# Optimization experiments

Measured on AMD Instinct MI355X. Metric: run time of the kernel, lower is better.

## Reference

```python
import jax, jax.numpy as jnp
import numpy as np

# AlphaFold-style Invariant Point Attention (the StructureModule's core op)
N, SD, PD, C, H, PQ, PV = 768, 384, 128, 16, 12, 4, 8
W_C = (2.0 / (9.0 * PQ)) ** 0.5   # point-distance weight
W_L = (1.0 / 3.0) ** 0.5          # logit balancing weight
INV_SQRT_C = C ** -0.5


def setup_inputs() -> dict:
    key = jax.random.key(0)
    ks = jax.random.split(key, 11)
    single_rep = jax.random.normal(ks[0], (N, SD), jnp.float32)
    pair_rep = jax.random.normal(ks[1], (N, N, PD), jnp.float32)
    # random rigid frames: proper orthonormal rotations via QR + translations
    M = jax.random.normal(ks[2], (N, 3, 3), jnp.float32)
    frames_R, _ = jnp.linalg.qr(M)
    frames_t = jax.random.normal(ks[3], (N, 3), jnp.float32) * 10.0
    s = 0.02
    W_qkv = jax.random.normal(ks[4], (SD, 3 * H * C), jnp.float32) * s
    W_b = jax.random.normal(ks[5], (PD, H), jnp.float32) * s
    W_qkp = jax.random.normal(ks[6], (SD, 2 * H * PQ * 3), jnp.float32) * s
    W_vp = jax.random.normal(ks[7], (SD, H * PV * 3), jnp.float32) * s
    gamma = jnp.zeros((H,), jnp.float32)
    W_out = jax.random.normal(ks[8], (H * (PD + C + 3 * PV + PV), SD), jnp.float32) * s
    b_out = jnp.zeros((SD,), jnp.float32)
    return dict(single_rep=single_rep, pair_rep=pair_rep, frames_R=frames_R,
                frames_t=frames_t, W_qkv=W_qkv, W_b=W_b, W_qkp=W_qkp,
                W_vp=W_vp, gamma=gamma, W_out=W_out, b_out=b_out)


def reference(single_rep, pair_rep, frames_R, frames_t,
              W_qkv, W_b, W_qkp, W_vp, gamma, W_out, b_out):
    n = single_rep.shape[0]
    # scalar q/k/v: [n, C, H] (module views as (proj_dim, n_heads))
    q, k, v = [x.reshape(n, C, H) for x in jnp.split(single_rep @ W_qkv, 3, axis=-1)]
    b = jnp.einsum('ijd,dh->ijh', pair_rep, W_b)             # pair bias [n,n,H]
    qp, kp = [x.reshape(n, PQ, 3, H) for x in jnp.split(single_rep @ W_qkp, 2, axis=-1)]
    vp = (single_rep @ W_vp).reshape(n, PV, 3, H)

    def to_global(p):  # apply frame T_i = (R_i, t_i) to local points
        return jnp.einsum('nxy,npyh->npxh', frames_R, p) + frames_t[:, None, :, None]

    qg, kg, vg = to_global(qp), to_global(kp), to_global(vp)

    # squared distances sum_p ||T_i q_p - T_j k_p||^2 without [n,n,PQ,3,H] temp
    sq = jnp.sum(qg * qg, axis=(1, 2))                       # [n,H]
    sk = jnp.sum(kg * kg, axis=(1, 2))                       # [n,H]
    cross = jnp.einsum('ipxh,jpxh->ijh', qg, kg)             # [n,n,H]
    dist2 = sq[:, None, :] + sk[None, :, :] - 2.0 * cross

    head_w = jax.nn.softplus(gamma)                          # per-head gamma
    logits = W_L * (INV_SQRT_C * jnp.einsum('ich,jch->ijh', q, k)
                    + b - 0.5 * W_C * head_w * dist2)
    attn = jax.nn.softmax(logits, axis=1)                    # softmax over j

    o_pair = jnp.einsum('ijh,ijd->ihd', attn, pair_rep)      # [n,H,PD]
    o = jnp.einsum('ijh,jch->ihc', attn, v)                  # [n,H,C]
    og = jnp.einsum('ijh,jpxh->ipxh', attn, vg)              # [n,PV,3,H]
    # back to local frame: R_i^T (og - t_i)
    ol = jnp.einsum('nyx,npyh->npxh', frames_R, og - frames_t[:, None, :, None])
    onorm = jnp.sqrt(jnp.sum(ol * ol, axis=2) + 1e-8)        # [n,PV,H]

    feats = jnp.concatenate([
        o_pair.reshape(n, -1),
        o.reshape(n, -1),
        jnp.moveaxis(ol, -1, 1).reshape(n, -1),
        jnp.moveaxis(onorm, -1, 1).reshape(n, -1)], axis=-1)  # [n, H*(PD+C+3PV+PV)]
    return feats @ W_out + b_out
```

## Files before the change

### kernel.cpp

```cpp
#include <hip/hip_runtime.h>
#include <hip/hip_bf16.h>

typedef float v4f __attribute__((ext_vector_type(4)));
typedef short bf8 __attribute__((ext_vector_type(8)));
typedef unsigned short u16;

constexpr float W_C_ = 0.23570226039551584f;
constexpr float W_L_ = 0.5773502691896258f;

__device__ __forceinline__ u16 f2bf(float f) {
  unsigned u = __float_as_uint(f);
  return (u16)((u + 0x7FFFu + ((u >> 16) & 1u)) >> 16);
}
__device__ __forceinline__ float bf2f(u16 h) {
  return __uint_as_float(((unsigned)h) << 16);
}
__device__ __forceinline__ float dot4(v4f a, v4f b) {
  return a.x * b.x + a.y * b.y + a.z * b.z + a.w * b.w;
}

__global__ __launch_bounds__(256) void convert_bf(const float* __restrict__ src,
                                                  u16* __restrict__ dst, int n8) {
  int idx = blockIdx.x * 256 + threadIdx.x;
  if (idx < n8) {
    v4f a = ((const v4f*)src)[idx * 2];
    v4f b = ((const v4f*)src)[idx * 2 + 1];
    bf8 o;
    o[0] = (short)f2bf(a.x); o[1] = (short)f2bf(a.y);
    o[2] = (short)f2bf(a.z); o[3] = (short)f2bf(a.w);
    o[4] = (short)f2bf(b.x); o[5] = (short)f2bf(b.y);
    o[6] = (short)f2bf(b.z); o[7] = (short)f2bf(b.w);
    ((bf8*)dst)[idx] = o;
  }
}

__global__ __launch_bounds__(256) void wfrag_k(const float* __restrict__ W,
                                               u16* __restrict__ frag,
                                               int K, int N) {
  __shared__ float Ws[32 * 384];
  const int ks = blockIdx.x, k0 = ks * 32, t = threadIdx.x;
  const int NTfull = (N + 15) >> 4;
  for (int n0 = 0; n0 < N; n0 += 384) {
    int PN = N - n0; if (PN > 384) PN = 384;
    __syncthreads();
    for (int idx = t; idx < 32 * PN; idx += 256) {
      int r = idx / PN, c = idx - r * PN;
      Ws[r * PN + c] = W[(size_t)(k0 + r) * N + n0 + c];
    }
    __syncthreads();
    int NTp = (PN + 15) >> 4;
    for (int c = t; c < NTp * 64; c += 256) {
      int nt = c >> 6, l = c & 63;
      int col = nt * 16 + (l & 15);
      bf8 o;
#pragma unroll
      for (int e = 0; e < 8; e++) {
        int rr = (l >> 4) * 8 + e;
        float f = (col < PN) ? Ws[rr * PN + col] : 0.f;
        o[e] = (short)f2bf(f);
      }
      ((bf8*)frag)[((size_t)ks * NTfull + (n0 >> 4) + nt) * 64 + l] = o;
    }
  }
}

__global__ __launch_bounds__(256) void gemm_f32(
    const float* __restrict__ A, const float* __restrict__ B,
    float* __restrict__ C, int M, int N, int K) {
  __shared__ float AsT[32][68];
  __shared__ float Bs[32][36];
  const int bi = blockIdx.y * 64, bj = blockIdx.x * 32;
  const int t = threadIdx.x, ty = t >> 4, tx = t & 15;
  v4f acc0 = {0.f, 0.f, 0.f, 0.f}, acc1 = {0.f, 0.f, 0.f, 0.f};
  for (int k0 = 0; k0 < K; k0 += 32) {
#pragma unroll
    for (int q = 0; q < 2; q++) {
      int idx = t + 256 * q;
      int row = idx >> 3, c4 = idx & 7;
      v4f av = *(const v4f*)(A + (size_t)(bi + row) * K + k0 + c4 * 4);
      AsT[c4 * 4 + 0][row] = av.x;
      AsT[c4 * 4 + 1][row] = av.y;
      AsT[c4 * 4 + 2][row] = av.z;
      AsT[c4 * 4 + 3][row] = av.w;
    }
    {
      int r = t >> 3, c4 = t & 7;
      *(v4f*)&Bs[r][c4 * 4] = *(const v4f*)(B + (size_t)(k0 + r) * N + bj + c4 * 4);
    }
    __syncthreads();
#pragma unroll
    for (int kk = 0; kk < 32; kk++) {
      v4f a = *(const v4f*)&AsT[kk][ty * 4];
      float b0 = Bs[kk][tx * 2], b1 = Bs[kk][tx * 2 + 1];
      acc0 += a * b0;
      acc1 += a * b1;
    }
    __syncthreads();
  }
#pragma unroll
  for (int e = 0; e < 4; e++) {
    int row = bi + ty * 4 + e;
    C[(size_t)row * N + bj + tx * 2] = acc0[e];
    C[(size_t)row * N + bj + tx * 2 + 1] = acc1[e];
  }
}

__global__ __launch_bounds__(256) void mfma_gemm(
    const u16* __restrict__ Abf, const u16* __restrict__ Bfrag,
    const float* __restrict__ bias, float* __restrict__ C,
    int M, int N, int K, int ldc) {
  __shared__ u16 As[64 * 32];
  const int t = threadIdx.x, w = t >> 6, l = t & 63;
  const int bi = blockIdx.y * 64, nt0 = blockIdx.x * 2;
  const int NT = N >> 4, KS = K >> 5;
  v4f acc0 = {0.f, 0.f, 0.f, 0.f}, acc1 = {0.f, 0.f, 0.f, 0.f};
  const int srow = t >> 2, sc = t & 3;
  const int wslot = (sc ^ (srow & 3)) * 8;
  const bf8* Bf = (const bf8*)Bfrag;

  bf8 areg = *(const bf8*)(Abf + (size_t)(bi + srow) * K + sc * 8);
  bf8 b0 = Bf[(size_t)(0 * NT + nt0) * 64 + l];
  bf8 b1 = Bf[(size_t)(0 * NT + nt0 + 1) * 64 + l];
  const int rdoff = (w * 16 + (l & 15)) * 32 + (((l >> 4) ^ (l & 3)) * 8);
  for (int ks = 0; ks < KS; ks++) {
    *(bf8*)&As[srow * 32 + wslot] = areg;
    bf8 an, bn0, bn1;
    if (ks + 1 < KS) {
      an = *(const bf8*)(Abf + (size_t)(bi + srow) * K + (ks + 1) * 32 + sc * 8);
      bn0 = Bf[(size_t)((ks + 1) * NT + nt0) * 64 + l];
      bn1 = Bf[(size_t)((ks + 1) * NT + nt0 + 1) * 64 + l];
    }
    __syncthreads();
    bf8 af = *(const bf8*)&As[rdoff];
    acc0 = __builtin_amdgcn_mfma_f32_16x16x32_bf16(af, b0, acc0, 0, 0, 0);
    acc1 = __builtin_amdgcn_mfma_f32_16x16x32_bf16(af, b1, acc1, 0, 0, 0);
    __syncthreads();
    areg = an; b0 = bn0; b1 = bn1;
  }
  int col0 = nt0 * 16 + (l & 15), col1 = col0 + 16;
  float bb0 = bias ? bias[col0] : 0.f;
  float bb1 = bias ? bias[col1] : 0.f;
#pragma unroll
  for (int r = 0; r < 4; r++) {
    int row = bi + w * 16 + (l >> 4) * 4 + r;
    C[(size_t)row * ldc + col0] = acc0[r] + bb0;
    C[(size_t)row * ldc + col1] = acc1[r] + bb1;
  }
}

__global__ __launch_bounds__(256) void prep_kernel(
    const float* __restrict__ projQKV, const float* __restrict__ projQKP,
    const float* __restrict__ projVP, const float* __restrict__ fR,
    const float* __restrict__ ft,
    float* __restrict__ qbuf, float* __restrict__ v2buf,
    float* __restrict__ qgbuf, float* __restrict__ sqbuf,
    float* __restrict__ kTT) {
  const int n = blockIdx.x, t = threadIdx.x;
  __shared__ float R[9], tt[3];
  __shared__ float qgL[144], kgL[144];
  if (t < 9) R[t] = fR[n * 9 + t];
  if (t < 3) tt[t] = ft[n * 3 + t];
  __syncthreads();
  const float* rQKV = projQKV + (size_t)n * 576;
  const float* rQKP = projQKP + (size_t)n * 288;
  const float* rVP = projVP + (size_t)n * 288;
  if (t < 192) {
    int h = t >> 4, c = t & 15;
    qbuf[(size_t)n * 192 + t] = rQKV[c * 12 + h];
    kTT[(size_t)(h * 29 + c) * 768 + n] = rQKV[192 + c * 12 + h];
    v2buf[(size_t)n * 480 + h * 40 + c] = rQKV[384 + c * 12 + h];
  }
  if (t < 144) {
    int e = t / 12, h = t % 12;
    int p = e / 3, x = e % 3;
    float aq = tt[x], ak = tt[x];
#pragma unroll
    for (int y = 0; y < 3; y++) {
      float r = R[x * 3 + y];
      aq += r * rQKP[p * 36 + y * 12 + h];
      ak += r * rQKP[144 + p * 36 + y * 12 + h];
    }
    qgL[h * 12 + e] = aq;
    kgL[h * 12 + e] = ak;
    qgbuf[(size_t)n * 144 + h * 12 + e] = aq;
    kTT[(size_t)(h * 29 + 16 + e) * 768 + n] = ak;
  }
  for (int idx = t; idx < 288; idx += 256) {
    int e = idx / 12, h = idx % 12;
    int p = e / 3, x = e % 3;
    float a = tt[x];
#pragma unroll
    for (int y = 0; y < 3; y++) a += R[x * 3 + y] * rVP[p * 36 + y * 12 + h];
    v2buf[(size_t)n * 480 + h * 40 + 16 + e] = a;
  }
  __syncthreads();
  if (t < 12) {
    float s = 0.f;
#pragma unroll
    for (int e = 0; e < 12; e++) { float v = qgL[t * 12 + e]; s += v * v; }
    sqbuf[n * 12 + t] = s;
  } else if (t < 24) {
    int h = t - 12;
    float s = 0.f;
#pragma unroll
    for (int e = 0; e < 12; e++) { float v = kgL[h * 12 + e]; s += v * v; }
    kTT[(size_t)(h * 29 + 28) * 768 + n] = s;
  }
}

__global__ __launch_bounds__(256) void bias_mfma(
    const float* __restrict__ pair, const u16* __restrict__ WbFrag,
    u16* __restrict__ bbuf) {
  const int jt = blockIdx.x, i = blockIdx.y;
  const int t = threadIdx.x, w = t >> 6, l = t & 63;
  __shared__ u16 pS[64 * 128];
  bf8 bf[4];
  const bf8* Wf = (const bf8*)WbFrag;
#pragma unroll
  for (int ks = 0; ks < 4; ks++) bf[ks] = Wf[ks * 64 + l];
  const float* pg = pair + ((size_t)i * 768 + jt * 64) * 128;
#pragma unroll
  for (int it = 0; it < 4; it++) {
    int idx = t + 256 * it;
    int j = idx >> 4, c = idx & 15;
    v4f x0 = *(const v4f*)(pg + j * 128 + c * 8);
    v4f x1 = *(const v4f*)(pg + j * 128 + c * 8 + 4);
    bf8 pk;
    pk[0] = (short)f2bf(x0.x); pk[1] = (short)f2bf(x0.y);
    pk[2] = (short)f2bf(x0.z); pk[3] = (short)f2bf(x0.w);
    pk[4] = (short)f2bf(x1.x); pk[5] = (short)f2bf(x1.y);
    pk[6] = (short)f2bf(x1.z); pk[7] = (short)f2bf(x1.w);
    *(bf8*)&pS[j * 128 + ((c ^ (j & 15)) * 8)] = pk;
  }
  __syncthreads();
  v4f acc = {0.f, 0.f, 0.f, 0.f};
#pragma unroll
  for (int ks = 0; ks < 4; ks++) {
    int slot = (ks * 4 + (l >> 4)) ^ (l & 15);
    bf8 af = *(const bf8*)&pS[(w * 16 + (l & 15)) * 128 + slot * 8];
    acc = __builtin_amdgcn_mfma_f32_16x16x32_bf16(af, bf[ks], acc, 0, 0, 0);
  }
  int h = l & 15;
  if (h < 12) {
    int jbase = jt * 64 + w * 16 + (l >> 4) * 4;
    u16* dst = bbuf + ((size_t)i * 12 + h) * 768 + jbase;
#pragma unroll
    for (int r = 0; r < 4; r++) dst[r] = f2bf(acc[r]);
  }
}

__global__ __launch_bounds__(256) void qk_softmax(
    const float* __restrict__ qbuf, const float* __restrict__ qgbuf,
    const float* __restrict__ sqbuf, const float* __restrict__ kTT,
    const u16* __restrict__ bbuf, const float* __restrict__ gamma,
    u16* __restrict__ attn) {
  const int h = blockIdx.x, i = blockIdx.y, t = threadIdx.x;
  __shared__ float red[8];
  float q[16], qg[12];
  const float* qb = qbuf + (size_t)i * 192 + h * 16;
  const float* qgb = qgbuf + (size_t)i * 144 + h * 12;
#pragma unroll
  for (int c = 0; c < 16; c++) q[c] = qb[c];
#pragma unroll
  for (int e = 0; e < 12; e++) qg[e] = qgb[e];
  float sq = sqbuf[i * 12 + h];
  float g = gamma[h];
  float hw = fmaxf(g, 0.f) + log1pf(expf(-fabsf(g)));
  const float* kb = kTT + (size_t)h * 29 * 768;
  const u16* brow = bbuf + ((size_t)i * 12 + h) * 768;
  float lg[3];
#pragma unroll
  for (int s = 0; s < 3; s++) {
    int j = t + 256 * s;
    float qk = 0.f;
#pragma unroll
    for (int c = 0; c < 16; c++) qk += q[c] * kb[c * 768 + j];
    float cr = 0.f;
#pragma unroll
    for (int e = 0; e < 12; e++) cr += qg[e] * kb[(16 + e) * 768 + j];
    float sk = kb[28 * 768 + j];
    float b = bf2f(brow[j]);
    float d2 = sq + sk - 2.f * cr;
    lg[s] = W_L_ * (0.25f * qk + b - 0.5f * W_C_ * hw * d2);
  }
  float m = fmaxf(fmaxf(lg[0], lg[1]), lg[2]);
#pragma unroll
  for (int o = 32; o >= 1; o >>= 1) m = fmaxf(m, __shfl_xor(m, o));
  if ((t & 63) == 0) red[t >> 6] = m;
  __syncthreads();
  m = fmaxf(fmaxf(red[0], red[1]), fmaxf(red[2], red[3]));
  float p0 = __expf(lg[0] - m), p1 = __expf(lg[1] - m), p2 = __expf(lg[2] - m);
  float ss = p0 + p1 + p2;
#pragma unroll
  for (int o = 32; o >= 1; o >>= 1) ss += __shfl_xor(ss, o);
  if ((t & 63) == 0) red[4 + (t >> 6)] = ss;
  __syncthreads();
  float inv = 1.f / (red[4] + red[5] + red[6] + red[7]);
  u16* arow = attn + ((size_t)i * 12 + h) * 768;
  arow[t] = f2bf(p0 * inv);
  arow[t + 256] = f2bf(p1 * inv);
  arow[t + 512] = f2bf(p2 * inv);
}

__global__ __launch_bounds__(256) void opair_k(
    const float* __restrict__ pair, const u16* __restrict__ attn,
    u16* __restrict__ feats_bf) {
  const int i = blockIdx.x, t = threadIdx.x;
  const int w = t >> 6, l = t & 63;
  const int dq = l & 31, hh = l >> 5;
  __shared__ float pairL[64][132];
  __shared__ float ALf[12][68];
  v4f acc[6];
#pragma unroll
  for (int k = 0; k < 6; k++) acc[k] = (v4f){0.f, 0.f, 0.f, 0.f};

  v4f pr[8];
  bf8 areg;
  {
    const float* pg = pair + ((size_t)i * 768) * 128;
#pragma unroll
    for (int it = 0; it < 8; it++) {
      int idx = t + 256 * it;
      pr[it] = *(const v4f*)(pg + (idx >> 5) * 128 + (idx & 31) * 4);
    }
    if (t < 96)
      areg = *(const bf8*)(attn + ((size_t)i * 12 + (t >> 3)) * 768 + (t & 7) * 8);
  }
  for (int jt = 0; jt < 12; jt++) {
#pragma unroll
    for (int it = 0; it < 8; it++) {
      int idx = t + 256 * it;
      *(v4f*)&pairL[idx >> 5][(idx & 31) * 4] = pr[it];
    }
    if (t < 96) {
      int hA = t >> 3, c = t & 7;
#pragma unroll
      for (int e = 0; e < 8; e++) ALf[hA][c * 8 + e] = bf2f((u16)areg[e]);
    }
    if (jt < 11) {
      const float* pg = pair + ((size_t)i * 768 + (jt + 1) * 64) * 128;
#pragma unroll
      for (int it = 0; it < 8; it++) {
        int idx = t + 256 * it;
        pr[it] = *(const v4f*)(pg + (idx >> 5) * 128 + (idx & 31) * 4);
      }
      if (t < 96)
        areg = *(const bf8*)(attn + ((size_t)i * 12 + (t >> 3)) * 768 +
                             (jt + 1) * 64 + (t & 7) * 8);
    }
    __syncthreads();
#pragma unroll
    for (int jj16 = 0; jj16 < 16; jj16++) {
      int jj = w * 16 + jj16;
      v4f pv = *(const v4f*)&pairL[jj][dq * 4];
      float a0 = ALf[hh * 6 + 0][jj];
      float a1 = ALf[hh * 6 + 1][jj];
      float a2 = ALf[hh * 6 + 2][jj];
      float a3 = ALf[hh * 6 + 3][jj];
      float a4 = ALf[hh * 6 + 4][jj];
      float a5 = ALf[hh * 6 + 5][jj];
      acc[0] += pv * a0; acc[1] += pv * a1; acc[2] += pv * a2;
      acc[3] += pv * a3; acc[4] += pv * a4; acc[5] += pv * a5;
    }
    __syncthreads();
  }
  float* red = &pairL[0][0];
#pragma unroll
  for (int k = 0; k < 6; k++)
    *(v4f*)&red[((w * 12 + hh * 6 + k) << 7) + dq * 4] = acc[k];
  __syncthreads();
  const size_t fb = (size_t)i * 2112;
#pragma unroll
  for (int s = 0; s < 6; s++) {
    int o = t + 256 * s;
    int ho = o >> 7, dd = o & 127;
    float v = red[(ho << 7) + dd] + red[((12 + ho) << 7) + dd] +
              red[((24 + ho) << 7) + dd] + red[((36 + ho) << 7) + dd];
    feats_bf[fb + o] = f2bf(v);
  }
}

__global__ __launch_bounds__(256) void ov_k(
    const u16* __restrict__ attn, const float* __restrict__ v2buf,
    float* __restrict__ O2) {
  const int i0 = blockIdx.x * 64, h = blockIdx.y, t = threadIdx.x;
  __shared__ float AL[64][65];
  __shared__ float VL[64][48];
  const int il = t & 63, eb = (t >> 6) * 12;
  v4f acc0 = {0.f, 0.f, 0.f, 0.f}, acc1 = {0.f, 0.f, 0.f, 0.f},
      acc2 = {0.f, 0.f, 0.f, 0.f};
  for (int jt = 0; jt < 12; ++jt) {
    const int j0 = jt * 64;
#pragma unroll
    for (int q = 0; q < 2; q++) {
      int idx = t + 256 * q;
      int ii = idx >> 3, c = idx & 7;
      bf8 av = *(const bf8*)(attn + ((size_t)(i0 + ii) * 12 + h) * 768 + j0 + c * 8);
#pragma unroll
      for (int e = 0; e < 8; e++) AL[ii][c * 8 + e] = bf2f((u16)av[e]);
    }
#pragma unroll
    for (int q = 0; q < 3; q++) {
      int idx = t + q * 256;
      if (idx < 640) {
        int jj = idx / 10, e4 = idx % 10;
        *(v4f*)&VL[jj][e4 * 4] =
            *(const v4f*)(v2buf + (size_t)(j0 + jj) * 480 + h * 40 + e4 * 4);
      }
    }
    __syncthreads();
#pragma unroll 4
    for (int jj = 0; jj < 64; ++jj) {
      float a = AL[il][jj];
      v4f v0 = *(const v4f*)&VL[jj][eb];
      v4f v1 = *(const v4f*)&VL[jj][eb + 4];
      v4f v2 = *(const v4f*)&VL[jj][eb + 8];
      acc0 += v0 * a;
      acc1 += v1 * a;
      acc2 += v2 * a;
    }
    __syncthreads();
  }
  float* orow = O2 + ((size_t)(i0 + il) * 12 + h) * 40;
#pragma unroll
  for (int s = 0; s < 12; ++s) {
    int e = eb + s;
    if (e < 40) {
      float v = (s < 4) ? ((float*)&acc0)[s]
                        : (s < 8) ? ((float*)&acc1)[s - 4] : ((float*)&acc2)[s - 8];
      orow[e] = v;
    }
  }
}

__global__ __launch_bounds__(256) void finalize_k(
    const float* __restrict__ O2, const float* __restrict__ fR,
    const float* __restrict__ ft, u16* __restrict__ feats_bf) {
  const int i = blockIdx.x, t = threadIdx.x;
  __shared__ float RL[9], ttL[3];
  if (t < 9) RL[t] = fR[i * 9 + t];
  if (t < 3) ttL[t] = ft[i * 3 + t];
  __syncthreads();
  const float* orow = O2 + (size_t)i * 480;
  const size_t fb = (size_t)i * 2112;
  if (t < 192) {
    int h = t >> 4, c = t & 15;
    feats_bf[fb + 1536 + h * 16 + c] = f2bf(orow[h * 40 + c]);
  }
  if (t < 96) {
    int h = t >> 3, p = t & 7;
    float og0 = orow[h * 40 + 16 + p * 3 + 0] - ttL[0];
    float og1 = orow[h * 40 + 16 + p * 3 + 1] - ttL[1];
    float og2 = orow[h * 40 + 16 + p * 3 + 2] - ttL[2];
    float o0 = RL[0] * og0 + RL[3] * og1 + RL[6] * og2;
    float o1 = RL[1] * og0 + RL[4] * og1 + RL[7] * og2;
    float o2 = RL[2] * og0 + RL[5] * og1 + RL[8] * og2;
    feats_bf[fb + 1728 + h * 24 + p * 3 + 0] = f2bf(o0);
    feats_bf[fb + 1728 + h * 24 + p * 3 + 1] = f2bf(o1);
    feats_bf[fb + 1728 + h * 24 + p * 3 + 2] = f2bf(o2);
    feats_bf[fb + 2016 + h * 8 + p] = f2bf(sqrtf(o0 * o0 + o1 * o1 + o2 * o2 + 1e-8f));
  }
}

extern "C" void kernel_launch(void* const* d_in, const int* in_sizes, int n_in,
                              void* d_out, int out_size, void* d_ws, size_t ws_size,
                              hipStream_t stream) {
  const float* single = (const float*)d_in[0];
  const float* pair = (const float*)d_in[1];
  const float* fR = (const float*)d_in[2];
  const float* ft = (const float*)d_in[3];
  const float* W_qkv = (const float*)d_in[4];
  const float* W_b = (const float*)d_in[5];
  const float* W_qkp = (const float*)d_in[6];
  const float* W_vp = (const float*)d_in[7];
  const float* gamma = (const float*)d_in[8];
  const float* W_out = (const float*)d_in[9];
  const float* b_out = (const float*)d_in[10];
  float* out = (float*)d_out;

  float* ws = (float*)d_ws;
  float* projQKV = ws;
  float* projQKP = projQKV + 442368;
  float* projVP  = projQKP + 221184;
  float* qbuf    = projVP + 221184;
  float* v2buf   = qbuf + 147456;
  float* qgbuf   = v2buf + 368640;
  float* sqbuf   = qgbuf + 110592;
  float* kTT     = sqbuf + 9216;
  float* O2      = kTT + 267264;
  u16* single_bf = (u16*)(O2 + 368640);
  u16* WqkvFrag  = single_bf + 294912;
  u16* WbFrag    = WqkvFrag + 221184;
  u16* WoutFrag  = WbFrag + 2048;
  u16* bbuf      = WoutFrag + 811008;
  u16* attn      = bbuf + 7077888;
  u16* feats_bf  = attn + 7077888;

  convert_bf<<<144, 256, 0, stream>>>(single, single_bf, 36864);
  wfrag_k<<<12, 256, 0, stream>>>(W_qkv, WqkvFrag, 384, 576);
  wfrag_k<<<4, 256, 0, stream>>>(W_b, WbFrag, 128, 12);
  wfrag_k<<<66, 256, 0, stream>>>(W_out, WoutFrag, 2112, 384);
  gemm_f32<<<dim3(9, 12), 256, 0, stream>>>(single, W_qkp, projQKP, 768, 288, 384);
  gemm_f32<<<dim3(9, 12), 256, 0, stream>>>(single, W_vp, projVP, 768, 288, 384);
  mfma_gemm<<<dim3(18, 12), 256, 0, stream>>>(single_bf, WqkvFrag, nullptr,
                                              projQKV, 768, 576, 384, 576);
  prep_kernel<<<768, 256, 0, stream>>>(projQKV, projQKP, projVP, fR, ft,
                                       qbuf, v2buf, qgbuf, sqbuf, kTT);
  bias_mfma<<<dim3(12, 768), 256, 0, stream>>>(pair, WbFrag, bbuf);
  qk_softmax<<<dim3(12, 768), 256, 0, stream>>>(qbuf, qgbuf, sqbuf, kTT, bbuf,
                                                gamma, attn);
  opair_k<<<768, 256, 0, stream>>>(pair, attn, feats_bf);
  ov_k<<<dim3(12, 12), 256, 0, stream>>>(attn, v2buf, O2);
  finalize_k<<<768, 256, 0, stream>>>(O2, fR, ft, feats_bf);
  mfma_gemm<<<dim3(12, 12), 256, 0, stream>>>(feats_bf, WoutFrag, b_out,
                                              out, 768, 384, 2112, 384);
}
```

Before: 310.6 us.

## Fuse pair bias with QK logits, cache bf16 pair copy, split softmax

The bias kernel now also computes the full logits (scalar QK, point-distance terms) per 64-column tile and writes them as fp32, while emitting a bf16 copy of pair_rep. A separate row softmax kernel then turns logits into bf16 attention, and opair reads the bf16 pair copy instead of re-reading fp32 pair. This halves the second large pair read in exchange for an extra bf16 write plus an fp32 logits round-trip. The point projections also move from fp32 SIMT GEMMs to bf16 MFMA GEMMs, which adds rounding error to the geometric terms.

```diff
diff --git a/kernel.cpp b/kernel.cpp
--- a/kernel.cpp
+++ b/kernel.cpp
@@ -36,7 +36,7 @@
 
 __global__ __launch_bounds__(256) void wfrag_k(const float* __restrict__ W,
                                                u16* __restrict__ frag,
-                                               int K, int N) {
+                                               int K, int N, float scale) {
   __shared__ float Ws[32 * 384];
   const int ks = blockIdx.x, k0 = ks * 32, t = threadIdx.x;
   const int NTfull = (N + 15) >> 4;
@@ -56,52 +56,11 @@
 #pragma unroll
       for (int e = 0; e < 8; e++) {
         int rr = (l >> 4) * 8 + e;
-        float f = (col < PN) ? Ws[rr * PN + col] : 0.f;
+        float f = (col < PN) ? Ws[rr * PN + col] * scale : 0.f;
         o[e] = (short)f2bf(f);
       }
       ((bf8*)frag)[((size_t)ks * NTfull + (n0 >> 4) + nt) * 64 + l] = o;
     }
-  }
-}
-
-__global__ __launch_bounds__(256) void gemm_f32(
-    const float* __restrict__ A, const float* __restrict__ B,
-    float* __restrict__ C, int M, int N, int K) {
-  __shared__ float AsT[32][68];
-  __shared__ float Bs[32][36];
-  const int bi = blockIdx.y * 64, bj = blockIdx.x * 32;
-  const int t = threadIdx.x, ty = t >> 4, tx = t & 15;
-  v4f acc0 = {0.f, 0.f, 0.f, 0.f}, acc1 = {0.f, 0.f, 0.f, 0.f};
-  for (int k0 = 0; k0 < K; k0 += 32) {
-#pragma unroll
-    for (int q = 0; q < 2; q++) {
-      int idx = t + 256 * q;
-      int row = idx >> 3, c4 = idx & 7;
-      v4f av = *(const v4f*)(A + (size_t)(bi + row) * K + k0 + c4 * 4);
-      AsT[c4 * 4 + 0][row] = av.x;
-      AsT[c4 * 4 + 1][row] = av.y;
-      AsT[c4 * 4 + 2][row] = av.z;
-      AsT[c4 * 4 + 3][row] = av.w;
-    }
-    {
-      int r = t >> 3, c4 = t & 7;
-      *(v4f*)&Bs[r][c4 * 4] = *(const v4f*)(B + (size_t)(k0 + r) * N + bj + c4 * 4);
-    }
-    __syncthreads();
-#pragma unroll
-    for (int kk = 0; kk < 32; kk++) {
-      v4f a = *(const v4f*)&AsT[kk][ty * 4];
-      float b0 = Bs[kk][tx * 2], b1 = Bs[kk][tx * 2 + 1];
-      acc0 += a * b0;
-      acc1 += a * b1;
-    }
-    __syncthreads();
-  }
-#pragma unroll
-  for (int e = 0; e < 4; e++) {
-    int row = bi + ty * 4 + e;
-    C[(size_t)row * N + bj + tx * 2] = acc0[e];
-    C[(size_t)row * N + bj + tx * 2 + 1] = acc1[e];
   }
 }
 
@@ -152,9 +111,9 @@
     const float* __restrict__ projQKV, const float* __restrict__ projQKP,
     const float* __restrict__ projVP, const float* __restrict__ fR,
     const float* __restrict__ ft,
-    float* __restrict__ qbuf, float* __restrict__ v2buf,
-    float* __restrict__ qgbuf, float* __restrict__ sqbuf,
-    float* __restrict__ kTT) {
+    float* __restrict__ qbuf, float* __restrict__ kbuf, float* __restrict__ v2buf,
+    float* __restrict__ qgbuf, float* __restrict__ kgbuf,
+    float* __restrict__ sqbuf, float* __restrict__ skbuf) {
   const int n = blockIdx.x, t = threadIdx.x;
   __shared__ float R[9], tt[3];
   __shared__ float qgL[144], kgL[144];
@@ -167,7 +126,7 @@
   if (t < 192) {
     int h = t >> 4, c = t & 15;
     qbuf[(size_t)n * 192 + t] = rQKV[c * 12 + h];
-    kTT[(size_t)(h * 29 + c) * 768 + n] = rQKV[192 + c * 12 + h];
+    kbuf[(size_t)n * 192 + t] = rQKV[192 + c * 12 + h];
     v2buf[(size_t)n * 480 + h * 40 + c] = rQKV[384 + c * 12 + h];
   }
   if (t < 144) {
@@ -183,7 +142,7 @@
     qgL[h * 12 + e] = aq;
     kgL[h * 12 + e] = ak;
     qgbuf[(size_t)n * 144 + h * 12 + e] = aq;
-    kTT[(size_t)(h * 29 + 16 + e) * 768 + n] = ak;
+    kgbuf[(size_t)n * 144 + h * 12 + e] = ak;
   }
   for (int idx = t; idx < 288; idx += 256) {
     int e = idx / 12, h = idx % 12;
@@ -204,21 +163,38 @@
     float s = 0.f;
 #pragma unroll
     for (int e = 0; e < 12; e++) { float v = kgL[h * 12 + e]; s += v * v; }
-    kTT[(size_t)(h * 29 + 28) * 768 + n] = s;
-  }
-}
-
-__global__ __launch_bounds__(256) void bias_mfma(
+    skbuf[n * 12 + h] = s;
+  }
+}
+
+__global__ __launch_bounds__(256) void biaslogit_k(
     const float* __restrict__ pair, const u16* __restrict__ WbFrag,
-    u16* __restrict__ bbuf) {
+    const float* __restrict__ gamma,
+    const float* __restrict__ qbuf, const float* __restrict__ kbuf,
+    const float* __restrict__ qgbuf, const float* __restrict__ kgbuf,
+    const float* __restrict__ sqbuf, const float* __restrict__ skbuf,
+    u16* __restrict__ pair_bf, float* __restrict__ logits) {
   const int jt = blockIdx.x, i = blockIdx.y;
   const int t = threadIdx.x, w = t >> 6, l = t & 63;
   __shared__ u16 pS[64 * 128];
-  bf8 bf[4];
+  __shared__ float lgL[64 * 15];
+  __shared__ float qL[192], qgL[144], c1L[12], c2L[12];
+
+  if (t < 192) qL[t] = qbuf[(size_t)i * 192 + t];
+  if (t < 144) qgL[t] = qgbuf[(size_t)i * 144 + t];
+  if (t < 12) {
+    float g = gamma[t];
+    float hw = fmaxf(g, 0.f) + log1pf(expf(-fabsf(g)));
+    c1L[t] = W_L_ * W_C_ * hw;
+    c2L[t] = -0.5f * c1L[t] * sqbuf[i * 12 + t];
+  }
+  bf8 wb[4];
   const bf8* Wf = (const bf8*)WbFrag;
 #pragma unroll
-  for (int ks = 0; ks < 4; ks++) bf[ks] = Wf[ks * 64 + l];
+  for (int ks = 0; ks < 4; ks++) wb[ks] = Wf[ks * 64 + l];
+
   const float* pg = pair + ((size_t)i * 768 + jt * 64) * 128;
+  u16* pbg = pair_bf + ((size_t)i * 768 + jt * 64) * 128;
 #pragma unroll
   for (int it = 0; it < 4; it++) {
     int idx = t + 256 * it;
@@ -231,118 +207,136 @@
     pk[4] = (short)f2bf(x1.x); pk[5] = (short)f2bf(x1.y);
     pk[6] = (short)f2bf(x1.z); pk[7] = (short)f2bf(x1.w);
     *(bf8*)&pS[j * 128 + ((c ^ (j & 15)) * 8)] = pk;
-  }
-  __syncthreads();
-  v4f acc = {0.f, 0.f, 0.f, 0.f};
-#pragma unroll
-  for (int ks = 0; ks < 4; ks++) {
-    int slot = (ks * 4 + (l >> 4)) ^ (l & 15);
-    bf8 af = *(const bf8*)&pS[(w * 16 + (l & 15)) * 128 + slot * 8];
-    acc = __builtin_amdgcn_mfma_f32_16x16x32_bf16(af, bf[ks], acc, 0, 0, 0);
-  }
-  int h = l & 15;
-  if (h < 12) {
-    int jbase = jt * 64 + w * 16 + (l >> 4) * 4;
-    u16* dst = bbuf + ((size_t)i * 12 + h) * 768 + jbase;
-#pragma unroll
-    for (int r = 0; r < 4; r++) dst[r] = f2bf(acc[r]);
-  }
-}
-
-__global__ __launch_bounds__(256) void qk_softmax(
-    const float* __restrict__ qbuf, const float* __restrict__ qgbuf,
-    const float* __restrict__ sqbuf, const float* __restrict__ kTT,
-    const u16* __restrict__ bbuf, const float* __restrict__ gamma,
-    u16* __restrict__ attn) {
-  const int h = blockIdx.x, i = blockIdx.y, t = threadIdx.x;
-  __shared__ float red[8];
-  float q[16], qg[12];
-  const float* qb = qbuf + (size_t)i * 192 + h * 16;
-  const float* qgb = qgbuf + (size_t)i * 144 + h * 12;
-#pragma unroll
-  for (int c = 0; c < 16; c++) q[c] = qb[c];
-#pragma unroll
-  for (int e = 0; e < 12; e++) qg[e] = qgb[e];
-  float sq = sqbuf[i * 12 + h];
-  float g = gamma[h];
-  float hw = fmaxf(g, 0.f) + log1pf(expf(-fabsf(g)));
-  const float* kb = kTT + (size_t)h * 29 * 768;
-  const u16* brow = bbuf + ((size_t)i * 12 + h) * 768;
-  float lg[3];
+    *(bf8*)(pbg + j * 128 + c * 8) = pk;
+  }
+  __syncthreads();
+
+  {
+    v4f acc = {0.f, 0.f, 0.f, 0.f};
+#pragma unroll
+    for (int ks = 0; ks < 4; ks++) {
+      int slot = (ks * 4 + (l >> 4)) ^ (l & 15);
+      bf8 af = *(const bf8*)&pS[(w * 16 + (l & 15)) * 128 + slot * 8];
+      acc = __builtin_amdgcn_mfma_f32_16x16x32_bf16(af, wb[ks], acc, 0, 0, 0);
+    }
+    int h = l & 15;
+    if (h < 12) {
+#pragma unroll
+      for (int r = 0; r < 4; r++)
+        lgL[(w * 16 + (l >> 4) * 4 + r) * 15 + h] = acc[r];
+    }
+  }
+  __syncthreads();
+
+  {
+    const int j = t >> 2, hg = t & 3;
+    const int jg = jt * 64 + j;
+#pragma unroll
+    for (int hh = 0; hh < 3; hh++) {
+      int h = hg * 3 + hh;
+      const v4f* kk = (const v4f*)(kbuf + (size_t)jg * 192 + h * 16);
+      const v4f* qq = (const v4f*)&qL[h * 16];
+      float qk = dot4(kk[0], qq[0]) + dot4(kk[1], qq[1]) +
+                 dot4(kk[2], qq[2]) + dot4(kk[3], qq[3]);
+      const v4f* kg = (const v4f*)(kgbuf + (size_t)jg * 144 + h * 12);
+      const v4f* qg = (const v4f*)&qgL[h * 12];
+      float cr = dot4(kg[0], qg[0]) + dot4(kg[1], qg[1]) + dot4(kg[2], qg[2]);
+      float sk = skbuf[(size_t)jg * 12 + h];
+      lgL[j * 15 + h] += 0.25f * W_L_ * qk + c1L[h] * (cr - 0.5f * sk) + c2L[h];
+    }
+  }
+  __syncthreads();
+
 #pragma unroll
   for (int s = 0; s < 3; s++) {
-    int j = t + 256 * s;
-    float qk = 0.f;
-#pragma unroll
-    for (int c = 0; c < 16; c++) qk += q[c] * kb[c * 768 + j];
-    float cr = 0.f;
-#pragma unroll
-    for (int e = 0; e < 12; e++) cr += qg[e] * kb[(16 + e) * 768 + j];
-    float sk = kb[28 * 768 + j];
-    float b = bf2f(brow[j]);
-    float d2 = sq + sk - 2.f * cr;
-    lg[s] = W_L_ * (0.25f * qk + b - 0.5f * W_C_ * hw * d2);
-  }
-  float m = fmaxf(fmaxf(lg[0], lg[1]), lg[2]);
-#pragma unroll
-  for (int o = 32; o >= 1; o >>= 1) m = fmaxf(m, __shfl_xor(m, o));
-  if ((t & 63) == 0) red[t >> 6] = m;
-  __syncthreads();
-  m = fmaxf(fmaxf(red[0], red[1]), fmaxf(red[2], red[3]));
-  float p0 = __expf(lg[0] - m), p1 = __expf(lg[1] - m), p2 = __expf(lg[2] - m);
-  float ss = p0 + p1 + p2;
-#pragma unroll
-  for (int o = 32; o >= 1; o >>= 1) ss += __shfl_xor(ss, o);
-  if ((t & 63) == 0) red[4 + (t >> 6)] = ss;
-  __syncthreads();
-  float inv = 1.f / (red[4] + red[5] + red[6] + red[7]);
-  u16* arow = attn + ((size_t)i * 12 + h) * 768;
-  arow[t] = f2bf(p0 * inv);
-  arow[t + 256] = f2bf(p1 * inv);
-  arow[t + 512] = f2bf(p2 * inv);
+    int o = t + 256 * s;
+    int h = o >> 6, j = o & 63;
+    logits[((size_t)i * 12 + h) * 768 + jt * 64 + j] = lgL[j * 15 + h];
+  }
+}
+
+__global__ __launch_bounds__(256) void softmax_bf(const float* __restrict__ L,
+                                                  u16* __restrict__ attn) {
+  const int row = blockIdx.x * 4 + (threadIdx.x >> 6);
+  const int lane = threadIdx.x & 63;
+  const v4f* p = (const v4f*)(L + (size_t)row * 768);
+  v4f a0 = p[lane], a1 = p[lane + 64], a2 = p[lane + 128];
+  float m0 = fmaxf(fmaxf(a0.x, a0.y), fmaxf(a0.z, a0.w));
+  float m1 = fmaxf(fmaxf(a1.x, a1.y), fmaxf(a1.z, a1.w));
+  float m2 = fmaxf(fmaxf(a2.x, a2.y), fmaxf(a2.z, a2.w));
+  float m = fmaxf(m0, fmaxf(m1, m2));
+#pragma unroll
+  for (int s = 32; s >= 1; s >>= 1) m = fmaxf(m, __shfl_xor(m, s));
+  a0.x = __expf(a0.x - m); a0.y = __expf(a0.y - m);
+  a0.z = __expf(a0.z - m); a0.w = __expf(a0.w - m);
+  a1.x = __expf(a1.x - m); a1.y = __expf(a1.y - m);
+  a1.z = __expf(a1.z - m); a1.w = __expf(a1.w - m);
+  a2.x = __expf(a2.x - m); a2.y = __expf(a2.y - m);
+  a2.z = __expf(a2.z - m); a2.w = __expf(a2.w - m);
+  float s = a0.x + a0.y + a0.z + a0.w + a1.x + a1.y + a1.z + a1.w +
+            a2.x + a2.y + a2.z + a2.w;
+#pragma unroll
+  for (int q = 32; q >= 1; q >>= 1) s += __shfl_xor(s, q);
+  float inv = 1.f / s;
+  a0 *= inv; a1 *= inv; a2 *= inv;
+  u16* arow = attn + (size_t)row * 768;
+  uint2 pk;
+  pk.x = (unsigned)f2bf(a0.x) | ((unsigned)f2bf(a0.y) << 16);
+  pk.y = (unsigned)f2bf(a0.z) | ((unsigned)f2bf(a0.w) << 16);
+  *(uint2*)&arow[lane * 4] = pk;
+  pk.x = (unsigned)f2bf(a1.x) | ((unsigned)f2bf(a1.y) << 16);
+  pk.y = (unsigned)f2bf(a1.z) | ((unsigned)f2bf(a1.w) << 16);
+  *(uint2*)&arow[256 + lane * 4] = pk;
+  pk.x = (unsigned)f2bf(a2.x) | ((unsigned)f2bf(a2.y) << 16);
+  pk.y = (unsigned)f2bf(a2.z) | ((unsigned)f2bf(a2.w) << 16);
+  *(uint2*)&arow[512 + lane * 4] = pk;
 }
 
 __global__ __launch_bounds__(256) void opair_k(
-    const float* __restrict__ pair, const u16* __restrict__ attn,
+    const u16* __restrict__ pair_bf, const u16* __restrict__ attn,
     u16* __restrict__ feats_bf) {
   const int i = blockIdx.x, t = threadIdx.x;
   const int w = t >> 6, l = t & 63;
   const int dq = l & 31, hh = l >> 5;
-  __shared__ float pairL[64][132];
-  __shared__ float ALf[12][68];
+  __shared__ float smemf[6160];
+  u16* pS = (u16*)smemf;
+  float* ALf = smemf + 4096;
+  float* red = smemf;
+
   v4f acc[6];
 #pragma unroll
   for (int k = 0; k < 6; k++) acc[k] = (v4f){0.f, 0.f, 0.f, 0.f};
 
-  v4f pr[8];
+  bf8 pr[4];
   bf8 areg;
   {
-    const float* pg = pair + ((size_t)i * 768) * 128;
-#pragma unroll
-    for (int it = 0; it < 8; it++) {
+    const u16* pg = pair_bf + (size_t)i * 768 * 128;
+#pragma unroll
+    for (int it = 0; it < 4; it++) {
       int idx = t + 256 * it;
-      pr[it] = *(const v4f*)(pg + (idx >> 5) * 128 + (idx & 31) * 4);
+      pr[it] = *(const bf8*)(pg + (idx >> 4) * 128 + (idx & 15) * 8);
     }
     if (t < 96)
       areg = *(const bf8*)(attn + ((size_t)i * 12 + (t >> 3)) * 768 + (t & 7) * 8);
   }
   for (int jt = 0; jt < 12; jt++) {
 #pragma unroll
-    for (int it = 0; it < 8; it++) {
+    for (int it = 0; it < 4; it++) {
       int idx = t + 256 * it;
-      *(v4f*)&pairL[idx >> 5][(idx & 31) * 4] = pr[it];
+      int j = idx >> 4, c = idx & 15;
+      *(bf8*)&pS[j * 128 + ((c ^ (j & 15)) * 8)] = pr[it];
     }
     if (t < 96) {
       int hA = t >> 3, c = t & 7;
 #pragma unroll
-      for (int e = 0; e < 8; e++) ALf[hA][c * 8 + e] = bf2f((u16)areg[e]);
+      for (int e = 0; e < 8; e++) ALf[hA * 68 + c * 8 + e] = bf2f((u16)areg[e]);
     }
     if (jt < 11) {
-      const float* pg = pair + ((size_t)i * 768 + (jt + 1) * 64) * 128;
-#pragma unroll
-      for (int it = 0; it < 8; it++) {
+      const u16* pg = pair_bf + ((size_t)i * 768 + (jt + 1) * 64) * 128;
+#pragma unroll
+      for (int it = 0; it < 4; it++) {
         int idx = t + 256 * it;
-        pr[it] = *(const v4f*)(pg + (idx >> 5) * 128 + (idx & 31) * 4);
+        pr[it] = *(const bf8*)(pg + (idx >> 4) * 128 + (idx & 15) * 8);
       }
       if (t < 96)
         areg = *(const bf8*)(attn + ((size_t)i * 12 + (t >> 3)) * 768 +
@@ -352,30 +346,32 @@
 #pragma unroll
     for (int jj16 = 0; jj16 < 16; jj16++) {
       int jj = w * 16 + jj16;
-      v4f pv = *(const v4f*)&pairL[jj][dq * 4];
-      float a0 = ALf[hh * 6 + 0][jj];
-      float a1 = ALf[hh * 6 + 1][jj];
-      float a2 = ALf[hh * 6 + 2][jj];
-      float a3 = ALf[hh * 6 + 3][jj];
-      float a4 = ALf[hh * 6 + 4][jj];
-      float a5 = ALf[hh * 6 + 5][jj];
+      const u16* pv4 = &pS[jj * 128 + (((dq >> 1) ^ (jj & 15)) * 8) + (dq & 1) * 4];
+      v4f pv;
+      pv.x = bf2f(pv4[0]); pv.y = bf2f(pv4[1]);
+      pv.z = bf2f(pv4[2]); pv.w = bf2f(pv4[3]);
+      float a0 = ALf[(hh * 6 + 0) * 68 + jj];
+      float a1 = ALf[(hh * 6 + 1) * 68 + jj];
+      float a2 = ALf[(hh * 6 + 2) * 68 + jj];
+      float a3 = ALf[(hh * 6 + 3) * 68 + jj];
+      float a4 = ALf[(hh * 6 + 4) * 68 + jj];
+      float a5 = ALf[(hh * 6 + 5) * 68 + jj];
       acc[0] += pv * a0; acc[1] += pv * a1; acc[2] += pv * a2;
       acc[3] += pv * a3; acc[4] += pv * a4; acc[5] += pv * a5;
     }
     __syncthreads();
   }
-  float* red = &pairL[0][0];
 #pragma unroll
   for (int k = 0; k < 6; k++)
-    *(v4f*)&red[((w * 12 + hh * 6 + k) << 7) + dq * 4] = acc[k];
+    *(v4f*)&red[(w * 12 + hh * 6 + k) * 128 + dq * 4] = acc[k];
   __syncthreads();
   const size_t fb = (size_t)i * 2112;
 #pragma unroll
   for (int s = 0; s < 6; s++) {
     int o = t + 256 * s;
     int ho = o >> 7, dd = o & 127;
-    float v = red[(ho << 7) + dd] + red[((12 + ho) << 7) + dd] +
-              red[((24 + ho) << 7) + dd] + red[((36 + ho) << 7) + dd];
+    float v = red[ho * 128 + dd] + red[(12 + ho) * 128 + dd] +
+              red[(24 + ho) * 128 + dd] + red[(36 + ho) * 128 + dd];
     feats_bf[fb + o] = f2bf(v);
   }
 }
@@ -480,36 +476,47 @@
 
   float* ws = (float*)d_ws;
   float* projQKV = ws;
-  float* projQKP = projQKV + 442368;
-  float* projVP  = projQKP + 221184;
-  float* qbuf    = projVP + 221184;
-  float* v2buf   = qbuf + 147456;
-  float* qgbuf   = v2buf + 368640;
-  float* sqbuf   = qgbuf + 110592;
-  float* kTT     = sqbuf + 9216;
-  float* O2      = kTT + 267264;
-  u16* single_bf = (u16*)(O2 + 368640);
-  u16* WqkvFrag  = single_bf + 294912;
-  u16* WbFrag    = WqkvFrag + 221184;
-  u16* WoutFrag  = WbFrag + 2048;
-  u16* bbuf      = WoutFrag + 811008;
-  u16* attn      = bbuf + 7077888;
-  u16* feats_bf  = attn + 7077888;
+  float* projQKP = ws + 442368;
+  float* projVP  = ws + 663552;
+  float* qbuf    = ws + 884736;
+  float* kbuf    = ws + 1032192;
+  float* v2buf   = ws + 1179648;
+  float* qgbuf   = ws + 1548288;
+  float* kgbuf   = ws + 1658880;
+  float* sqbuf   = ws + 1769472;
+  float* skbuf   = ws + 1778688;
+  float* logits  = ws + 1787904;
+  float* O2      = ws + 8865792;
+  u16* ub        = (u16*)(ws + 9234432);
+  u16* single_bf = ub;
+  u16* WqkvFrag  = ub + 294912;
+  u16* WqkpFrag  = ub + 516096;
+  u16* WvpFrag   = ub + 626688;
+  u16* WbFrag    = ub + 737280;
+  u16* WoutFrag  = ub + 739328;
+  u16* attn      = ub + 1550336;
+  u16* feats_bf  = ub + 8628224;
+  u16* pair_bf   = ub + 10250240;
 
   convert_bf<<<144, 256, 0, stream>>>(single, single_bf, 36864);
-  wfrag_k<<<12, 256, 0, stream>>>(W_qkv, WqkvFrag, 384, 576);
-  wfrag_k<<<4, 256, 0, stream>>>(W_b, WbFrag, 128, 12);
-  wfrag_k<<<66, 256, 0, stream>>>(W_out, WoutFrag, 2112, 384);
-  gemm_f32<<<dim3(9, 12), 256, 0, stream>>>(single, W_qkp, projQKP, 768, 288, 384);
-  gemm_f32<<<dim3(9, 12), 256, 0, stream>>>(single, W_vp, projVP, 768, 288, 384);
+  wfrag_k<<<12, 256, 0, stream>>>(W_qkv, WqkvFrag, 384, 576, 1.f);
+  wfrag_k<<<12, 256, 0, stream>>>(W_qkp, WqkpFrag, 384, 288, 1.f);
+  wfrag_k<<<12, 256, 0, stream>>>(W_vp, WvpFrag, 384, 288, 1.f);
+  wfrag_k<<<4, 256, 0, stream>>>(W_b, WbFrag, 128, 12, W_L_);
+  wfrag_k<<<66, 256, 0, stream>>>(W_out, WoutFrag, 2112, 384, 1.f);
   mfma_gemm<<<dim3(18, 12), 256, 0, stream>>>(single_bf, WqkvFrag, nullptr,
                                               projQKV, 768, 576, 384, 576);
+  mfma_gemm<<<dim3(9, 12), 256, 0, stream>>>(single_bf, WqkpFrag, nullptr,
+                                             projQKP, 768, 288, 384, 288);
+  mfma_gemm<<<dim3(9, 12), 256, 0, stream>>>(single_bf, WvpFrag, nullptr,
+                                             projVP, 768, 288, 384, 288);
   prep_kernel<<<768, 256, 0, stream>>>(projQKV, projQKP, projVP, fR, ft,
-                                       qbuf, v2buf, qgbuf, sqbuf, kTT);
-  bias_mfma<<<dim3(12, 768), 256, 0, stream>>>(pair, WbFrag, bbuf);
-  qk_softmax<<<dim3(12, 768), 256, 0, stream>>>(qbuf, qgbuf, sqbuf, kTT, bbuf,
-                                                gamma, attn);
-  opair_k<<<768, 256, 0, stream>>>(pair, attn, feats_bf);
+                                       qbuf, kbuf, v2buf, qgbuf, kgbuf, sqbuf, skbuf);
+  biaslogit_k<<<dim3(12, 768), 256, 0, stream>>>(pair, WbFrag, gamma, qbuf, kbuf,
+                                                 qgbuf, kgbuf, sqbuf, skbuf,
+                                                 pair_bf, logits);
+  softmax_bf<<<2304, 256, 0, stream>>>(logits, attn);
+  opair_k<<<768, 256, 0, stream>>>(pair_bf, attn, feats_bf);
   ov_k<<<dim3(12, 12), 256, 0, stream>>>(attn, v2buf, O2);
   finalize_k<<<768, 256, 0, stream>>>(O2, fR, ft, feats_bf);
   mfma_gemm<<<dim3(12, 12), 256, 0, stream>>>(feats_bf, WoutFrag, b_out,
```

Result: slower. 353.0 us (+13.7%).
